# Kernel optimization log

Measured on AMD Instinct MI355X. Metric: run time of the kernel, lower is better.

The kernel has to match this reference:

```python
import jax, jax.numpy as jnp
import numpy as np

SEQ, B, IN, H, L = 1024, 64, 256, 512, 2
EPS = 1e-5


def setup_inputs() -> dict:
    key = jax.random.key(0)
    ks = jax.random.split(key, 4)
    x = jax.random.normal(ks[0], (SEQ, B, IN), dtype=jnp.float32)
    h0 = jnp.zeros((L, B, H), dtype=jnp.float32)
    c0 = jnp.zeros((L, B, H), dtype=jnp.float32)
    # torch Linear weight layout: [4*H, in_features]
    W0 = jax.random.normal(ks[1], (4 * H, IN + H), dtype=jnp.float32) * 0.05
    b0 = jnp.zeros((4 * H,), dtype=jnp.float32)
    W1 = jax.random.normal(ks[2], (4 * H, H + H), dtype=jnp.float32) * 0.05
    b1 = jnp.zeros((4 * H,), dtype=jnp.float32)
    g0 = jnp.ones((H,), dtype=jnp.float32)
    beta0 = jnp.zeros((H,), dtype=jnp.float32)
    g1 = jnp.ones((H,), dtype=jnp.float32)
    beta1 = jnp.zeros((H,), dtype=jnp.float32)
    return {"x": x, "h0": h0, "c0": c0, "W0": W0, "b0": b0, "g0": g0,
            "beta0": beta0, "W1": W1, "b1": b1, "g1": g1, "beta1": beta1}


def _layer_norm(z, g, b):
    mu = jnp.mean(z, axis=-1, keepdims=True)
    var = jnp.mean(jnp.square(z - mu), axis=-1, keepdims=True)
    return (z - mu) * jax.lax.rsqrt(var + EPS) * g + b


def _cell(inp, h, c, W, b, g, beta):
    # gates: [B, 4H] via Linear on concat(x, h)
    gates = jnp.concatenate([inp, h], axis=-1) @ W.T + b
    i_t, f_t, o_t, cand = jnp.split(gates, 4, axis=-1)
    i_t = jax.nn.sigmoid(i_t)
    f_t = jax.nn.sigmoid(f_t)
    o_t = jax.nn.sigmoid(o_t)
    cand = jnp.tanh(cand)
    c_new = i_t * cand + f_t * c
    h_new = o_t * jnp.tanh(_layer_norm(c_new, g, beta))
    return h_new, c_new


def reference(x, h0, c0, W0, b0, g0, beta0, W1, b1, g1, beta1):
    def step(carry, xt):
        ha, ca, hb, cb = carry
        ha, ca = _cell(xt, ha, ca, W0, b0, g0, beta0)
        hb, cb = _cell(ha, hb, cb, W1, b1, g1, beta1)
        return (ha, ca, hb, cb), hb

    carry0 = (h0[0], c0[0], h0[1], c0[1])
    (ha, ca, hb, cb), outputs = jax.lax.scan(step, carry0, x)
    h_final = jnp.stack([ha, hb])  # [L, B, H]
    c_final = jnp.stack([ca, cb])
    return outputs, h_final, c_final
```

## Files before the change

kernel.cpp:

```cpp
#include <hip/hip_runtime.h>


typedef short  s16x8 __attribute__((ext_vector_type(8)));
typedef float  f32x4 __attribute__((ext_vector_type(4)));
typedef float  f32x2 __attribute__((ext_vector_type(2)));
typedef unsigned short u16;
typedef unsigned int   u32;
typedef unsigned long long u64;

constexpr int kSeq = 1024;

constexpr size_t OF_FLAGS = 0;
constexpr size_t OF_STAT0 = 1024;
constexpr size_t OF_STAT1 = 17408;
constexpr size_t OF_HA    = 33792;
constexpr size_t OF_HB    = 164864;
constexpr size_t OF_W0S   = 295936;
constexpr size_t OF_W1S   = 3441664;
constexpr size_t OF_XBF   = 7635968;
constexpr size_t WS_NEED  = OF_XBF + 33554432;

constexpr size_t OUT_HFIN = (size_t)kSeq * 64 * 512;
constexpr size_t OUT_CFIN = OUT_HFIN + 2 * 64 * 512;

__device__ __forceinline__ u16 f2bf(float f) {
  u32 u = __float_as_uint(f);
  return (u16)((u + 0x7fffu + ((u >> 16) & 1u)) >> 16);
}

__device__ __forceinline__ void ldg16_coh(s16x8& d, const void* p) {
  asm volatile("global_load_dwordx4 %0, %1, off sc0 sc1" : "=v"(d) : "v"(p) : "memory");
}
__device__ __forceinline__ void ldg8f_coh(f32x2& d, const void* p) {
  asm volatile("global_load_dwordx2 %0, %1, off sc0 sc1" : "=v"(d) : "v"(p) : "memory");
}
__device__ __forceinline__ void stg8_coh(float* p, float a, float b) {
  f32x2 t; t[0] = a; t[1] = b;
  asm volatile("global_store_dwordx2 %0, %1, off sc0 sc1" :: "v"(p), "v"(t) : "memory");
}
__device__ __forceinline__ void stg2_coh(u16* p, u32 v) {
  asm volatile("global_store_short %0, %1, off sc0 sc1" :: "v"(p), "v"(v) : "memory");
}
__device__ __forceinline__ void vm_wait() {
  asm volatile("s_waitcnt vmcnt(0)" ::: "memory");
  __builtin_amdgcn_sched_barrier(0);
}
__device__ __forceinline__ void waitge(u32* f, u32 tgt) {
  const int l = threadIdx.x & 31;
  while (true) {
    u32 v = __hip_atomic_load(&f[l], __ATOMIC_RELAXED, __HIP_MEMORY_SCOPE_AGENT);
    if (__all((int)(v >= tgt))) break;
    __builtin_amdgcn_s_sleep(2);
  }
}

__global__ void conv_x_k(const float* __restrict__ x, u16* __restrict__ xd, size_t n) {
  size_t i = (size_t)blockIdx.x * blockDim.x + threadIdx.x;
  size_t st = (size_t)gridDim.x * blockDim.x;
  for (; i < n; i += st) xd[i] = f2bf(x[i]);
}

__global__ void conv_w_k(const float* __restrict__ W, u16* __restrict__ Wd,
                         int KST, int Kdim) {
  int i = blockIdx.x * blockDim.x + threadIdx.x;
  if (i >= 32 * KST * 2048) return;
  int e = i & 7, lane = (i >> 3) & 63, nt = (i >> 9) & 3;
  int r = i >> 11;
  int kst = r % KST, ns = r / KST;
  int n_orig = nt * 512 + ns * 16 + (lane & 15);
  int k = kst * 32 + ((lane >> 4) << 3) + e;
  Wd[i] = f2bf(W[(size_t)n_orig * Kdim + k]);
}

__global__ void init_k(char* ws, const float* __restrict__ h0) {
  int i = blockIdx.x * blockDim.x + threadIdx.x;
  u32* f = (u32*)ws;
  if (i < 64) f[i] = 0u;
  if (i < 4096) {
    ((u64*)(ws + OF_STAT0))[i] = 0x8000000000000000ull;
    ((u64*)(ws + OF_STAT1))[i] = 0x8000000000000000ull;
  }
  ((u16*)(ws + OF_HA))[32768 + i] = f2bf(h0[i]);
  ((u16*)(ws + OF_HB))[32768 + i] = f2bf(h0[32768 + i]);
}

template <int ROLE>
__device__ __forceinline__ void team_loop(
    int ns, char* smem,
    const u16* __restrict__ xbf, const u16* __restrict__ wsw,
    u16* hA, u16* hB, float* statT, u32* flags,
    const float* __restrict__ bias, const float* __restrict__ gam_,
    const float* __restrict__ bet_, const float* __restrict__ c0in,
    float* __restrict__ out)
{
  constexpr int KST = ROLE ? 32 : 24;
  const int tid = threadIdx.x;
  const int lane = tid & 63, wid = tid >> 6;
  const int arow = wid * 16 + (lane & 15);
  const int acol = (lane >> 4) << 3;
  const int jl = tid & 15, rg = tid >> 4;
  const int jg = ns * 16 + jl;

  u32* HFA = flags;
  u32* HF1 = flags + 32;
  u32* HF  = ROLE ? HF1 : HFA;

  s16x8* wl    = (s16x8*)smem;
  float* gates = (float*)(smem + (size_t)KST * 4096);
  float* mus   = (float*)(smem + (size_t)KST * 4096 + 17408);

  const s16x8* wsrc = (const s16x8*)wsw + (size_t)ns * KST * 256;
  for (int i = tid; i < KST * 256; i += 256) wl[i] = wsrc[i];

  const float bi = bias[jg], bf_ = bias[512 + jg], bo = bias[1024 + jg], bc = bias[1536 + jg];
  const float gm = gam_[jg], bt = bet_[jg];
  float cst[4];
  #pragma unroll
  for (int k = 0; k < 4; ++k)
    cst[k] = c0in[(size_t)(ROLE * 64 + rg * 4 + k) * 512 + jg];
  __syncthreads();

  for (int t = 0; t < kSeq; ++t) {
    f32x4 acc[4];
    #pragma unroll
    for (int nt = 0; nt < 4; ++nt) acc[nt] = (f32x4){0.f, 0.f, 0.f, 0.f};

    if (ROLE == 0) {
      s16x8 xp[8];
      const u16* xr = xbf + ((size_t)t * 64 + arow) * 256 + acol;
      #pragma unroll
      for (int kk = 0; kk < 8; ++kk) xp[kk] = *(const s16x8*)(xr + kk * 32);
      if (wid == 0)      { if (t > 0)  waitge(HFA, (u32)t); }
      else if (wid == 1) { if (t >= 2) waitge(HF1, (u32)(t - 1)); }
      __syncthreads();
      s16x8 a[16];
      const u16* hr = hA + (size_t)((t + 1) & 1) * 32768 + (size_t)arow * 512 + acol;
      #pragma unroll
      for (int kk = 0; kk < 16; ++kk) ldg16_coh(a[kk], hr + kk * 32);
      #pragma unroll
      for (int kk = 0; kk < 8; ++kk)
        #pragma unroll
        for (int nt = 0; nt < 4; ++nt)
          acc[nt] = __builtin_amdgcn_mfma_f32_16x16x32_bf16(xp[kk], wl[(kk * 4 + nt) * 64 + lane], acc[nt], 0, 0, 0);
      vm_wait();
      #pragma unroll
      for (int kk = 0; kk < 16; ++kk)
        #pragma unroll
        for (int nt = 0; nt < 4; ++nt)
          acc[nt] = __builtin_amdgcn_mfma_f32_16x16x32_bf16(a[kk], wl[((8 + kk) * 4 + nt) * 64 + lane], acc[nt], 0, 0, 0);
    } else {
      if (wid == 0) { if (t > 0) waitge(HF1, (u32)t); }
      __syncthreads();
      s16x8 a[16];
      const u16* hbr = hB + (size_t)((t + 1) & 1) * 32768 + (size_t)arow * 512 + acol;
      #pragma unroll
      for (int kk = 0; kk < 16; ++kk) ldg16_coh(a[kk], hbr + kk * 32);
      vm_wait();
      #pragma unroll
      for (int kk = 0; kk < 16; ++kk)
        #pragma unroll
        for (int nt = 0; nt < 4; ++nt)
          acc[nt] = __builtin_amdgcn_mfma_f32_16x16x32_bf16(a[kk], wl[((16 + kk) * 4 + nt) * 64 + lane], acc[nt], 0, 0, 0);
      if (wid == 0) waitge(HFA, (u32)(t + 1));
      __syncthreads();
      const u16* har = hA + (size_t)(t & 1) * 32768 + (size_t)arow * 512 + acol;
      #pragma unroll
      for (int kk = 0; kk < 16; ++kk) ldg16_coh(a[kk], har + kk * 32);
      vm_wait();
      #pragma unroll
      for (int kk = 0; kk < 16; ++kk)
        #pragma unroll
        for (int nt = 0; nt < 4; ++nt)
          acc[nt] = __builtin_amdgcn_mfma_f32_16x16x32_bf16(a[kk], wl[(kk * 4 + nt) * 64 + lane], acc[nt], 0, 0, 0);
    }

    #pragma unroll
    for (int nt = 0; nt < 4; ++nt) {
      const int brow = wid * 16 + ((lane >> 4) << 2);
      #pragma unroll
      for (int r = 0; r < 4; ++r)
        gates[(nt * 64 + brow + r) * 17 + (lane & 15)] = acc[nt][r];
    }
    __syncthreads();

    float cc[4], oo[4], sv[4], qv[4];
    #pragma unroll
    for (int k = 0; k < 4; ++k) {
      const int row = rg * 4 + k;
      const float gi = gates[(0 * 64 + row) * 17 + jl] + bi;
      const float gf = gates[(1 * 64 + row) * 17 + jl] + bf_;
      const float go = gates[(2 * 64 + row) * 17 + jl] + bo;
      const float gc = gates[(3 * 64 + row) * 17 + jl] + bc;
      const float iv = 1.f / (1.f + __expf(-gi));
      const float fv = 1.f / (1.f + __expf(-gf));
      oo[k] = 1.f / (1.f + __expf(-go));
      const float cn = iv * tanhf(gc) + fv * cst[k];
      cst[k] = cn; cc[k] = cn;
      sv[k] = cn; qv[k] = cn * cn;
    }
    #pragma unroll
    for (int m = 1; m <= 8; m <<= 1)
      #pragma unroll
      for (int k = 0; k < 4; ++k) { sv[k] += __shfl_xor(sv[k], m); qv[k] += __shfl_xor(qv[k], m); }
    if (jl == 0) {
      #pragma unroll
      for (int k = 0; k < 4; ++k) {
        const int row = rg * 4 + k;
        const float qs = (t & 1) ? -qv[k] : qv[k];
        stg8_coh(statT + ((size_t)row * 32 + ns) * 2, sv[k], qs);
      }
    }

    {
      const float* base = statT + (((size_t)(tid >> 2) * 32) + (size_t)(tid & 3) * 8) * 2;
      const u32 want = (u32)(t & 1);
      f32x2 e[8];
      while (true) {
        #pragma unroll
        for (int j = 0; j < 8; ++j) ldg8f_coh(e[j], base + j * 2);
        vm_wait();
        bool ok = true;
        #pragma unroll
        for (int j = 0; j < 8; ++j) ok &= ((__float_as_uint(e[j][1]) >> 31) == want);
        if (__all((int)ok)) break;
        __builtin_amdgcn_s_sleep(1);
      }
      float ss = 0.f, qq = 0.f;
      #pragma unroll
      for (int j = 0; j < 8; ++j) { ss += e[j][0]; qq += __builtin_fabsf(e[j][1]); }
      ss += __shfl_xor(ss, 1); qq += __shfl_xor(qq, 1);
      ss += __shfl_xor(ss, 2); qq += __shfl_xor(qq, 2);
      if ((lane & 3) == 0) {
        const int row = tid >> 2;
        const float mu = ss * (1.f / 512.f);
        const float ms = qq * (1.f / 512.f);
        mus[row * 2] = mu;
        mus[row * 2 + 1] = rsqrtf(ms - mu * mu + 1e-5f);
      }
    }

    #pragma unroll
    for (int k = 0; k < 4; ++k) {
      const int row = rg * 4 + k;
      const float mu = mus[row * 2], rs = mus[row * 2 + 1];
      const float hv = oo[k] * tanhf((cc[k] - mu) * rs * gm + bt);
      const u32 h16 = f2bf(hv);
      if (ROLE == 0) {
        stg2_coh(hA + (size_t)(t & 1) * 32768 + (size_t)row * 512 + jg, h16);
      } else {
        stg2_coh(hB + (size_t)(t & 1) * 32768 + (size_t)row * 512 + jg, h16);
        out[((size_t)t * 64 + row) * 512 + jg] = hv;
      }
      if (t == kSeq - 1) {
        out[OUT_HFIN + (size_t)ROLE * 32768 + (size_t)row * 512 + jg] = hv;
        out[OUT_CFIN + (size_t)ROLE * 32768 + (size_t)row * 512 + jg] = cc[k];
      }
    }
    vm_wait();
    __syncthreads();
    if (tid == 0)
      __hip_atomic_store(&HF[ns], (u32)(t + 1), __ATOMIC_RELAXED, __HIP_MEMORY_SCOPE_AGENT);
  }
}

__global__ __launch_bounds__(256, 1) void lstm_persist(
    const u16* __restrict__ xbf, const u16* __restrict__ w0s, const u16* __restrict__ w1s,
    char* ws,
    const float* __restrict__ b0, const float* __restrict__ lg0, const float* __restrict__ lb0,
    const float* __restrict__ b1, const float* __restrict__ lg1, const float* __restrict__ lb1,
    const float* __restrict__ c0in, float* __restrict__ out)
{
  extern __shared__ char smem[];
  const int bid = blockIdx.x;
  u32*   flags = (u32*)(ws + OF_FLAGS);
  u16*   hA    = (u16*)(ws + OF_HA);
  u16*   hB    = (u16*)(ws + OF_HB);
  float* st0   = (float*)(ws + OF_STAT0);
  float* st1   = (float*)(ws + OF_STAT1);

  if (bid < 32)
    team_loop<0>(bid, smem, xbf, w0s, hA, hB, st0, flags, b0, lg0, lb0, c0in, out);
  else
    team_loop<1>(bid - 32, smem, xbf, w1s, hA, hB, st1, flags, b1, lg1, lb1, c0in, out);
}

extern "C" void kernel_launch(void* const* d_in, const int* in_sizes, int n_in,
                              void* d_out, int out_size, void* d_ws, size_t ws_size,
                              hipStream_t stream) {
  (void)in_sizes; (void)n_in; (void)out_size;
  const float* x   = (const float*)d_in[0];
  const float* h0  = (const float*)d_in[1];
  const float* c0  = (const float*)d_in[2];
  const float* W0  = (const float*)d_in[3];
  const float* b0  = (const float*)d_in[4];
  const float* g0  = (const float*)d_in[5];
  const float* be0 = (const float*)d_in[6];
  const float* W1  = (const float*)d_in[7];
  const float* b1  = (const float*)d_in[8];
  const float* g1  = (const float*)d_in[9];
  const float* be1 = (const float*)d_in[10];
  float* out = (float*)d_out;

  if (ws_size < WS_NEED) return;

  char* ws = (char*)d_ws;
  u16* w0s = (u16*)(ws + OF_W0S);
  u16* w1s = (u16*)(ws + OF_W1S);
  u16* xbf = (u16*)(ws + OF_XBF);

  hipLaunchKernelGGL(conv_x_k, dim3(2048), dim3(256), 0, stream,
                     x, xbf, (size_t)kSeq * 64 * 256);
  hipLaunchKernelGGL(conv_w_k, dim3(6144), dim3(256), 0, stream, W0, w0s, 24, 768);
  hipLaunchKernelGGL(conv_w_k, dim3(8192), dim3(256), 0, stream, W1, w1s, 32, 1024);
  hipLaunchKernelGGL(init_k,   dim3(128),  dim3(256), 0, stream, ws, h0);
  hipLaunchKernelGGL(lstm_persist, dim3(64), dim3(256), 148992, stream,
                     xbf, w0s, w1s, ws,
                     b0, g0, be0, b1, g1, be1, c0, out);
}
```

Measured before the change: 15.83 ms.

## Tag hidden states with parity bits to replace flag polling with per-wave readiness

Result: slower. 37.61 ms (+137.5%).

```diff
diff --git a/kernel.cpp b/kernel.cpp
--- a/kernel.cpp
+++ b/kernel.cpp
@@ -11,13 +11,13 @@
 constexpr int kSeq = 1024;
 
 constexpr size_t OF_FLAGS = 0;
-constexpr size_t OF_STAT0 = 1024;
-constexpr size_t OF_STAT1 = 17408;
-constexpr size_t OF_HA    = 33792;
-constexpr size_t OF_HB    = 164864;
-constexpr size_t OF_W0S   = 295936;
-constexpr size_t OF_W1S   = 3441664;
-constexpr size_t OF_XBF   = 7635968;
+constexpr size_t OF_STAT0 = 2048;
+constexpr size_t OF_STAT1 = 18432;
+constexpr size_t OF_HA    = 34816;
+constexpr size_t OF_HB    = 296960;
+constexpr size_t OF_W0S   = 559104;
+constexpr size_t OF_W1S   = 3704832;
+constexpr size_t OF_XBF   = 7899136;
 constexpr size_t WS_NEED  = OF_XBF + 33554432;
 
 constexpr size_t OUT_HFIN = (size_t)kSeq * 64 * 512;
@@ -28,7 +28,7 @@
   return (u16)((u + 0x7fffu + ((u >> 16) & 1u)) >> 16);
 }
 
-__device__ __forceinline__ void ldg16_coh(s16x8& d, const void* p) {
+__device__ __forceinline__ void ldg16f_coh(f32x4& d, const void* p) {
   asm volatile("global_load_dwordx4 %0, %1, off sc0 sc1" : "=v"(d) : "v"(p) : "memory");
 }
 __device__ __forceinline__ void ldg8f_coh(f32x2& d, const void* p) {
@@ -38,19 +38,67 @@
   f32x2 t; t[0] = a; t[1] = b;
   asm volatile("global_store_dwordx2 %0, %1, off sc0 sc1" :: "v"(p), "v"(t) : "memory");
 }
-__device__ __forceinline__ void stg2_coh(u16* p, u32 v) {
-  asm volatile("global_store_short %0, %1, off sc0 sc1" :: "v"(p), "v"(v) : "memory");
+__device__ __forceinline__ void stg4_coh(float* p, u32 v) {
+  asm volatile("global_store_dword %0, %1, off sc0 sc1" :: "v"(p), "v"(v) : "memory");
 }
 __device__ __forceinline__ void vm_wait() {
   asm volatile("s_waitcnt vmcnt(0)" ::: "memory");
   __builtin_amdgcn_sched_barrier(0);
 }
-__device__ __forceinline__ void waitge(u32* f, u32 tgt) {
+__device__ __forceinline__ void waitge32(u32* f, u32 tgt) {
   const int l = threadIdx.x & 31;
   while (true) {
     u32 v = __hip_atomic_load(&f[l], __ATOMIC_RELAXED, __HIP_MEMORY_SCOPE_AGENT);
     if (__all((int)(v >= tgt))) break;
     __builtin_amdgcn_s_sleep(2);
+  }
+}
+
+__device__ __forceinline__ s16x8 frag_from(f32x4 a, f32x4 b) {
+  #pragma unroll
+  for (int e = 0; e < 4; ++e) {
+    a[e] = __uint_as_float(__float_as_uint(a[e]) & 0xBFFFFFFFu);
+    b[e] = __uint_as_float(__float_as_uint(b[e]) & 0xBFFFFFFFu);
+  }
+  union { u32 w[4]; s16x8 s; } r;
+  asm("v_cvt_pk_bf16_f32 %0, %1, %2" : "=v"(r.w[0]) : "v"(a[0]), "v"(a[1]));
+  asm("v_cvt_pk_bf16_f32 %0, %1, %2" : "=v"(r.w[1]) : "v"(a[2]), "v"(a[3]));
+  asm("v_cvt_pk_bf16_f32 %0, %1, %2" : "=v"(r.w[2]) : "v"(b[0]), "v"(b[1]));
+  asm("v_cvt_pk_bf16_f32 %0, %1, %2" : "=v"(r.w[3]) : "v"(b[2]), "v"(b[3]));
+  return r.s;
+}
+
+__device__ __forceinline__ void acquire_h(
+    f32x4 (&u)[16][2], const float* hrow, u32 wantT, u32* flagArr, u32 flagTgt)
+{
+  auto load_all = [&]() {
+    #pragma unroll
+    for (int kk = 0; kk < 16; ++kk) {
+      ldg16f_coh(u[kk][0], hrow + kk * 32);
+      ldg16f_coh(u[kk][1], hrow + kk * 32 + 4);
+    }
+  };
+  load_all();
+  int tries = 0; bool ok = false;
+  while (true) {
+    vm_wait();
+    u32 bad = 0;
+    #pragma unroll
+    for (int kk = 0; kk < 16; ++kk)
+      #pragma unroll
+      for (int j = 0; j < 2; ++j)
+        #pragma unroll
+        for (int e = 0; e < 4; ++e)
+          bad |= ((__float_as_uint(u[kk][j][e]) >> 30) ^ wantT) & 1u;
+    if (__all((int)(bad == 0))) { ok = true; break; }
+    if (++tries >= 16) break;
+    __builtin_amdgcn_s_sleep(1);
+    load_all();
+  }
+  if (!ok) {
+    waitge32(flagArr, flagTgt);
+    load_all();
+    vm_wait();
   }
 }
 
@@ -75,20 +123,27 @@
 __global__ void init_k(char* ws, const float* __restrict__ h0) {
   int i = blockIdx.x * blockDim.x + threadIdx.x;
   u32* f = (u32*)ws;
-  if (i < 64) f[i] = 0u;
-  if (i < 4096) {
+  if (i < 384) f[i] = 0u;
+  if (i < 2048) {
     ((u64*)(ws + OF_STAT0))[i] = 0x8000000000000000ull;
     ((u64*)(ws + OF_STAT1))[i] = 0x8000000000000000ull;
   }
-  ((u16*)(ws + OF_HA))[32768 + i] = f2bf(h0[i]);
-  ((u16*)(ws + OF_HB))[32768 + i] = f2bf(h0[32768 + i]);
+  float* hAf = (float*)(ws + OF_HA);
+  float* hBf = (float*)(ws + OF_HB);
+  u32 bA = (__float_as_uint(h0[i])         & 0xBFFFFFFFu) | 0x40000000u;
+  u32 bB = (__float_as_uint(h0[32768 + i]) & 0xBFFFFFFFu) | 0x40000000u;
+  hAf[32768 + i] = __uint_as_float(bA);
+  hBf[32768 + i] = __uint_as_float(bB);
+  hAf[i] = __uint_as_float(0x40000000u);
+  hBf[i] = __uint_as_float(0x40000000u);
 }
 
 template <int ROLE>
 __device__ __forceinline__ void team_loop(
     int ns, char* smem,
     const u16* __restrict__ xbf, const u16* __restrict__ wsw,
-    u16* hA, u16* hB, float* statT, u32* flags,
+    float* hAf, float* hBf, float* statT,
+    u32* HFA, u32* HFB, u32* BP,
     const float* __restrict__ bias, const float* __restrict__ gam_,
     const float* __restrict__ bet_, const float* __restrict__ c0in,
     float* __restrict__ out)
@@ -98,128 +153,119 @@
   const int lane = tid & 63, wid = tid >> 6;
   const int arow = wid * 16 + (lane & 15);
   const int acol = (lane >> 4) << 3;
-  const int jl = tid & 15, rg = tid >> 4;
-  const int jg = ns * 16 + jl;
-
-  u32* HFA = flags;
-  u32* HF1 = flags + 32;
-  u32* HF  = ROLE ? HF1 : HFA;
-
-  s16x8* wl    = (s16x8*)smem;
-  float* gates = (float*)(smem + (size_t)KST * 4096);
-  float* mus   = (float*)(smem + (size_t)KST * 4096 + 17408);
+  const int colL = lane & 15;
+  const int jgl  = ns * 16 + colL;
+  const int rbase = wid * 16 + ((lane >> 4) << 2);
+
+  u32* HF = ROLE ? HFB : HFA;
+
+  s16x8* wl  = (s16x8*)smem;
+  float* mus = (float*)(smem + (size_t)KST * 4096);
 
   const s16x8* wsrc = (const s16x8*)wsw + (size_t)ns * KST * 256;
   for (int i = tid; i < KST * 256; i += 256) wl[i] = wsrc[i];
 
-  const float bi = bias[jg], bf_ = bias[512 + jg], bo = bias[1024 + jg], bc = bias[1536 + jg];
-  const float gm = gam_[jg], bt = bet_[jg];
+  const float bi = bias[jgl], bf_ = bias[512 + jgl];
+  const float bo = bias[1024 + jgl], bc = bias[1536 + jgl];
+  const float gm = gam_[jgl], bt = bet_[jgl];
   float cst[4];
   #pragma unroll
   for (int k = 0; k < 4; ++k)
-    cst[k] = c0in[(size_t)(ROLE * 64 + rg * 4 + k) * 512 + jg];
+    cst[k] = c0in[(size_t)(ROLE * 64 + rbase + k) * 512 + jgl];
   __syncthreads();
 
   for (int t = 0; t < kSeq; ++t) {
+    const u32 tagPub = ((u32)t >> 1) & 1;
+    if (ROLE == 0 && t >= 2) waitge32(BP + wid * 32, (u32)(t - 1));
+
     f32x4 acc[4];
     #pragma unroll
     for (int nt = 0; nt < 4; ++nt) acc[nt] = (f32x4){0.f, 0.f, 0.f, 0.f};
+    f32x4 u[16][2];
 
     if (ROLE == 0) {
       s16x8 xp[8];
       const u16* xr = xbf + ((size_t)t * 64 + arow) * 256 + acol;
       #pragma unroll
       for (int kk = 0; kk < 8; ++kk) xp[kk] = *(const s16x8*)(xr + kk * 32);
-      if (wid == 0)      { if (t > 0)  waitge(HFA, (u32)t); }
-      else if (wid == 1) { if (t >= 2) waitge(HF1, (u32)(t - 1)); }
-      __syncthreads();
-      s16x8 a[16];
-      const u16* hr = hA + (size_t)((t + 1) & 1) * 32768 + (size_t)arow * 512 + acol;
-      #pragma unroll
-      for (int kk = 0; kk < 16; ++kk) ldg16_coh(a[kk], hr + kk * 32);
       #pragma unroll
       for (int kk = 0; kk < 8; ++kk)
         #pragma unroll
         for (int nt = 0; nt < 4; ++nt)
-          acc[nt] = __builtin_amdgcn_mfma_f32_16x16x32_bf16(xp[kk], wl[(kk * 4 + nt) * 64 + lane], acc[nt], 0, 0, 0);
-      vm_wait();
-      #pragma unroll
-      for (int kk = 0; kk < 16; ++kk)
+          acc[nt] = __builtin_amdgcn_mfma_f32_16x16x32_bf16(
+              xp[kk], wl[(kk * 4 + nt) * 64 + lane], acc[nt], 0, 0, 0);
+      acquire_h(u, hAf + (size_t)((t + 1) & 1) * 32768 + (size_t)arow * 512 + acol,
+                ((u32)(t - 1) >> 1) & 1, HFA + wid * 32, (u32)t);
+      #pragma unroll
+      for (int kk = 0; kk < 16; ++kk) {
+        s16x8 af = frag_from(u[kk][0], u[kk][1]);
         #pragma unroll
         for (int nt = 0; nt < 4; ++nt)
-          acc[nt] = __builtin_amdgcn_mfma_f32_16x16x32_bf16(a[kk], wl[((8 + kk) * 4 + nt) * 64 + lane], acc[nt], 0, 0, 0);
+          acc[nt] = __builtin_amdgcn_mfma_f32_16x16x32_bf16(
+              af, wl[((8 + kk) * 4 + nt) * 64 + lane], acc[nt], 0, 0, 0);
+      }
     } else {
-      if (wid == 0) { if (t > 0) waitge(HF1, (u32)t); }
-      __syncthreads();
-      s16x8 a[16];
-      const u16* hbr = hB + (size_t)((t + 1) & 1) * 32768 + (size_t)arow * 512 + acol;
-      #pragma unroll
-      for (int kk = 0; kk < 16; ++kk) ldg16_coh(a[kk], hbr + kk * 32);
-      vm_wait();
-      #pragma unroll
-      for (int kk = 0; kk < 16; ++kk)
+      acquire_h(u, hBf + (size_t)((t + 1) & 1) * 32768 + (size_t)arow * 512 + acol,
+                ((u32)(t - 1) >> 1) & 1, HFB + wid * 32, (u32)t);
+      #pragma unroll
+      for (int kk = 0; kk < 16; ++kk) {
+        s16x8 af = frag_from(u[kk][0], u[kk][1]);
         #pragma unroll
         for (int nt = 0; nt < 4; ++nt)
-          acc[nt] = __builtin_amdgcn_mfma_f32_16x16x32_bf16(a[kk], wl[((16 + kk) * 4 + nt) * 64 + lane], acc[nt], 0, 0, 0);
-      if (wid == 0) waitge(HFA, (u32)(t + 1));
-      __syncthreads();
-      const u16* har = hA + (size_t)(t & 1) * 32768 + (size_t)arow * 512 + acol;
-      #pragma unroll
-      for (int kk = 0; kk < 16; ++kk) ldg16_coh(a[kk], har + kk * 32);
-      vm_wait();
-      #pragma unroll
-      for (int kk = 0; kk < 16; ++kk)
+          acc[nt] = __builtin_amdgcn_mfma_f32_16x16x32_bf16(
+              af, wl[((16 + kk) * 4 + nt) * 64 + lane], acc[nt], 0, 0, 0);
+      }
+      acquire_h(u, hAf + (size_t)(t & 1) * 32768 + (size_t)arow * 512 + acol,
+                ((u32)t >> 1) & 1, HFA + wid * 32, (u32)(t + 1));
+      if (lane == 0)
+        __hip_atomic_store(&BP[wid * 32 + ns], (u32)(t + 1),
+                           __ATOMIC_RELAXED, __HIP_MEMORY_SCOPE_AGENT);
+      #pragma unroll
+      for (int kk = 0; kk < 16; ++kk) {
+        s16x8 af = frag_from(u[kk][0], u[kk][1]);
         #pragma unroll
         for (int nt = 0; nt < 4; ++nt)
-          acc[nt] = __builtin_amdgcn_mfma_f32_16x16x32_bf16(a[kk], wl[(kk * 4 + nt) * 64 + lane], acc[nt], 0, 0, 0);
-    }
-
-    #pragma unroll
-    for (int nt = 0; nt < 4; ++nt) {
-      const int brow = wid * 16 + ((lane >> 4) << 2);
-      #pragma unroll
-      for (int r = 0; r < 4; ++r)
-        gates[(nt * 64 + brow + r) * 17 + (lane & 15)] = acc[nt][r];
-    }
-    __syncthreads();
-
-    float cc[4], oo[4], sv[4], qv[4];
+          acc[nt] = __builtin_amdgcn_mfma_f32_16x16x32_bf16(
+              af, wl[(kk * 4 + nt) * 64 + lane], acc[nt], 0, 0, 0);
+      }
+    }
+
+    float oo[4], sv[4], qv[4];
     #pragma unroll
     for (int k = 0; k < 4; ++k) {
-      const int row = rg * 4 + k;
-      const float gi = gates[(0 * 64 + row) * 17 + jl] + bi;
-      const float gf = gates[(1 * 64 + row) * 17 + jl] + bf_;
-      const float go = gates[(2 * 64 + row) * 17 + jl] + bo;
-      const float gc = gates[(3 * 64 + row) * 17 + jl] + bc;
+      const float gi = acc[0][k] + bi;
+      const float gf = acc[1][k] + bf_;
+      const float go = acc[2][k] + bo;
+      const float gc = acc[3][k] + bc;
       const float iv = 1.f / (1.f + __expf(-gi));
       const float fv = 1.f / (1.f + __expf(-gf));
       oo[k] = 1.f / (1.f + __expf(-go));
       const float cn = iv * tanhf(gc) + fv * cst[k];
-      cst[k] = cn; cc[k] = cn;
+      cst[k] = cn;
       sv[k] = cn; qv[k] = cn * cn;
     }
     #pragma unroll
     for (int m = 1; m <= 8; m <<= 1)
       #pragma unroll
       for (int k = 0; k < 4; ++k) { sv[k] += __shfl_xor(sv[k], m); qv[k] += __shfl_xor(qv[k], m); }
-    if (jl == 0) {
+    if (colL == 0) {
       #pragma unroll
       for (int k = 0; k < 4; ++k) {
-        const int row = rg * 4 + k;
         const float qs = (t & 1) ? -qv[k] : qv[k];
-        stg8_coh(statT + ((size_t)row * 32 + ns) * 2, sv[k], qs);
+        stg8_coh(statT + ((size_t)(rbase + k) * 32 + ns) * 2, sv[k], qs);
       }
     }
 
     {
-      const float* base = statT + (((size_t)(tid >> 2) * 32) + (size_t)(tid & 3) * 8) * 2;
+      const int prow = wid * 16 + (lane >> 2);
+      const float* pb = statT + ((size_t)prow * 32 + (size_t)(lane & 3) * 8) * 2;
       const u32 want = (u32)(t & 1);
       f32x2 e[8];
       while (true) {
         #pragma unroll
-        for (int j = 0; j < 8; ++j) ldg8f_coh(e[j], base + j * 2);
+        for (int j = 0; j < 8; ++j) ldg8f_coh(e[j], pb + j * 2);
         vm_wait();
-        bool ok = true;
+        u32 ok = 1;
         #pragma unroll
         for (int j = 0; j < 8; ++j) ok &= ((__float_as_uint(e[j][1]) >> 31) == want);
         if (__all((int)ok)) break;
@@ -231,35 +277,40 @@
       ss += __shfl_xor(ss, 1); qq += __shfl_xor(qq, 1);
       ss += __shfl_xor(ss, 2); qq += __shfl_xor(qq, 2);
       if ((lane & 3) == 0) {
-        const int row = tid >> 2;
         const float mu = ss * (1.f / 512.f);
         const float ms = qq * (1.f / 512.f);
-        mus[row * 2] = mu;
-        mus[row * 2 + 1] = rsqrtf(ms - mu * mu + 1e-5f);
-      }
-    }
-
+        mus[prow * 2]     = mu;
+        mus[prow * 2 + 1] = rsqrtf(fmaxf(ms - mu * mu, 0.f) + 1e-5f);
+      }
+    }
+
+    float* hdst = (ROLE ? hBf : hAf) + (size_t)(t & 1) * 32768;
+    float hvv[4];
     #pragma unroll
     for (int k = 0; k < 4; ++k) {
-      const int row = rg * 4 + k;
+      const int row = rbase + k;
       const float mu = mus[row * 2], rs = mus[row * 2 + 1];
-      const float hv = oo[k] * tanhf((cc[k] - mu) * rs * gm + bt);
-      const u32 h16 = f2bf(hv);
-      if (ROLE == 0) {
-        stg2_coh(hA + (size_t)(t & 1) * 32768 + (size_t)row * 512 + jg, h16);
-      } else {
-        stg2_coh(hB + (size_t)(t & 1) * 32768 + (size_t)row * 512 + jg, h16);
-        out[((size_t)t * 64 + row) * 512 + jg] = hv;
-      }
-      if (t == kSeq - 1) {
-        out[OUT_HFIN + (size_t)ROLE * 32768 + (size_t)row * 512 + jg] = hv;
-        out[OUT_CFIN + (size_t)ROLE * 32768 + (size_t)row * 512 + jg] = cc[k];
+      const float hv = oo[k] * tanhf((cst[k] - mu) * rs * gm + bt);
+      hvv[k] = hv;
+      stg4_coh(hdst + (size_t)row * 512 + jgl,
+               (__float_as_uint(hv) & 0xBFFFFFFFu) | (tagPub << 30));
+    }
+    if (ROLE == 1) {
+      #pragma unroll
+      for (int k = 0; k < 4; ++k)
+        out[((size_t)t * 64 + rbase + k) * 512 + jgl] = hvv[k];
+    }
+    if (t == kSeq - 1) {
+      #pragma unroll
+      for (int k = 0; k < 4; ++k) {
+        out[OUT_HFIN + (size_t)ROLE * 32768 + (size_t)(rbase + k) * 512 + jgl] = hvv[k];
+        out[OUT_CFIN + (size_t)ROLE * 32768 + (size_t)(rbase + k) * 512 + jgl] = cst[k];
       }
     }
     vm_wait();
-    __syncthreads();
-    if (tid == 0)
-      __hip_atomic_store(&HF[ns], (u32)(t + 1), __ATOMIC_RELAXED, __HIP_MEMORY_SCOPE_AGENT);
+    if (lane == 0)
+      __hip_atomic_store(&HF[wid * 32 + ns], (u32)(t + 1),
+                         __ATOMIC_RELAXED, __HIP_MEMORY_SCOPE_AGENT);
   }
 }
 
@@ -272,16 +323,20 @@
 {
   extern __shared__ char smem[];
   const int bid = blockIdx.x;
-  u32*   flags = (u32*)(ws + OF_FLAGS);
-  u16*   hA    = (u16*)(ws + OF_HA);
-  u16*   hB    = (u16*)(ws + OF_HB);
-  float* st0   = (float*)(ws + OF_STAT0);
-  float* st1   = (float*)(ws + OF_STAT1);
+  u32* HFA = (u32*)(ws + OF_FLAGS);
+  u32* HFB = HFA + 128;
+  u32* BP  = HFA + 256;
+  float* hAf = (float*)(ws + OF_HA);
+  float* hBf = (float*)(ws + OF_HB);
+  float* st0 = (float*)(ws + OF_STAT0);
+  float* st1 = (float*)(ws + OF_STAT1);
 
   if (bid < 32)
-    team_loop<0>(bid, smem, xbf, w0s, hA, hB, st0, flags, b0, lg0, lb0, c0in, out);
+    team_loop<0>(bid, smem, xbf, w0s, hAf, hBf, st0, HFA, HFB, BP,
+                 b0, lg0, lb0, c0in, out);
   else
-    team_loop<1>(bid - 32, smem, xbf, w1s, hA, hB, st1, flags, b1, lg1, lb1, c0in, out);
+    team_loop<1>(bid - 32, smem, xbf, w1s, hAf, hBf, st1, HFA, HFB, BP,
+                 b1, lg1, lb1, c0in, out);
 }
 
 extern "C" void kernel_launch(void* const* d_in, const int* in_sizes, int n_in,
@@ -313,7 +368,7 @@
   hipLaunchKernelGGL(conv_w_k, dim3(6144), dim3(256), 0, stream, W0, w0s, 24, 768);
   hipLaunchKernelGGL(conv_w_k, dim3(8192), dim3(256), 0, stream, W1, w1s, 32, 1024);
   hipLaunchKernelGGL(init_k,   dim3(128),  dim3(256), 0, stream, ws, h0);
-  hipLaunchKernelGGL(lstm_persist, dim3(64), dim3(256), 148992, stream,
+  hipLaunchKernelGGL(lstm_persist, dim3(64), dim3(256), 131584, stream,
                      xbf, w0s, w1s, ws,
                      b0, g0, be0, b1, g1, be1, c0, out);
 }
```
